# Performance work log

Hardware: AMD Instinct MI355X
Metric: run time of the kernel (lower is better)

The kernel has to match this reference:

```python
import jax, jax.numpy as jnp
import numpy as np

T = 2048      # sequence length (single unbatched sequence)
V = 32000     # vocab
D = 1024      # d_model
E = 16        # number of experts (one structural group)
TOPK = 2      # router top-k
CAP = 256     # per-expert capacity (T*TOPK/E)
DFF = 2048    # expert MLP hidden
NHOPS = 2     # number of routing hops
EPS = 1e-5    # RMSNorm eps


def setup_inputs() -> dict:
    key = jax.random.key(0)
    ks = jax.random.split(key, 6)
    ids = jax.random.randint(ks[0], (T,), 0, V)
    embed_W = jax.random.normal(ks[1], (V, D), jnp.float32) * 0.02
    ln_scale = jnp.ones((D,), jnp.float32)
    router_W = jax.random.normal(ks[2], (NHOPS, D, E), jnp.float32) * (D ** -0.5)
    expert_W1 = jax.random.normal(ks[3], (NHOPS, E, D, DFF), jnp.float32) * (D ** -0.5)
    expert_W2 = jax.random.normal(ks[4], (NHOPS, E, DFF, D), jnp.float32) * (DFF ** -0.5)
    return dict(ids=ids, embed_W=embed_W, ln_scale=ln_scale,
                router_W=router_W, expert_W1=expert_W1, expert_W2=expert_W2)


def _hop(h, Wr, W1, W2):
    # Router: clean logits -> mixing probs (softmax) + hard top-k selection mask.
    logits = h @ Wr                                   # (T, E)
    probs = jax.nn.softmax(logits, axis=-1)           # (T, E)
    _, top = jax.lax.top_k(logits, TOPK)              # (T, TOPK)
    mask = jnp.zeros((T, E), bool).at[jnp.arange(T)[:, None], top].set(True)

    # _capacity_select: rank tokens per expert by clean logits, keep top CAP.
    m = mask.T                                        # (E, T)
    g = jnp.where(m, logits.T, -jnp.inf)              # (E, T)
    _, top_idx = jax.lax.top_k(g, CAP)                # (E, C)
    slot = jnp.zeros((E, CAP, T), h.dtype)
    slot = slot.at[jnp.arange(E)[:, None], jnp.arange(CAP)[None, :], top_idx].set(1.0)
    slot = slot * m[:, None, :].astype(h.dtype)       # zero slots filled from -inf
    kept = slot.sum(1) > 0                            # (E, T)

    # One-hot einsum gather of token states into expert slot buffers.
    xin = jnp.einsum('ect,td->ecd', slot, h)          # (E, C, D)

    # Stable sort slots by original token position (active slots first).
    active = slot.sum(-1) > 0                         # (E, C)
    pos = jnp.where(active, top_idx, T + 1)
    order = jnp.argsort(pos, axis=1, stable=True)     # (E, C)
    xin = jnp.take_along_axis(xin, order[:, :, None], axis=1)
    slot = jnp.take_along_axis(slot, order[:, :, None], axis=1)

    # Grouped (stacked/vmapped) expert execution: GELU MLP per expert.
    h1 = jax.nn.gelu(jnp.einsum('ecd,edf->ecf', xin, W1))
    expert_out = jnp.einsum('ecf,efd->ecd', h1, W2)   # (E, C, D)

    # Combine (Eq. 3): h_{s+1} = h_s + sum_e rho_e (M_e(h) - h)
    cw = jnp.where(kept.T, probs, 0.0)                # (T, E)
    rho = cw.sum(axis=1, keepdims=True)               # (T, 1)
    combine = jnp.einsum('ecd,ect,et->td', expert_out, slot, cw.T)
    return h + combine - rho * h


def reference(ids, embed_W, ln_scale, router_W, expert_W1, expert_W2):
    h = embed_W[ids]                                  # (T, D) embedding lookup
    for i in range(NHOPS):
        h = _hop(h, router_W[i], expert_W1[i], expert_W2[i])
    # RMSNorm + tied unembedding
    h = h * jax.lax.rsqrt(jnp.mean(h * h, axis=-1, keepdims=True) + EPS) * ln_scale
    return h @ embed_W.T                              # (T, V)
```

## Files before the change

kernel.cpp:

```cpp
#include <hip/hip_runtime.h>
#include <stdint.h>

#define T_ 2048
#define V_ 32000
#define D_ 1024
#define E_ 16
#define CAP_ 256
#define DFF_ 2048

typedef unsigned short u16;
typedef unsigned int u32;
typedef __bf16 bf16x8 __attribute__((ext_vector_type(8)));
typedef float f32x4 __attribute__((ext_vector_type(4)));

__device__ __forceinline__ u16 f2bf(float f){
  u32 u = __float_as_uint(f);
  u32 r = u + 0x7FFFu + ((u >> 16) & 1u);
  return (u16)(r >> 16);
}
__device__ __forceinline__ float bf2f(u16 s){ return __uint_as_float(((u32)s) << 16); }

__device__ __forceinline__ void gl_lds16(const void* g, void* l){
  __builtin_amdgcn_global_load_lds((const __attribute__((address_space(1))) void*)g,
                                   (__attribute__((address_space(3))) void*)l, 16, 0, 0);
}
__device__ __forceinline__ f32x4 mfma16(bf16x8 a, bf16x8 b, f32x4 c){
  return __builtin_amdgcn_mfma_f32_16x16x32_bf16(a, b, c, 0, 0, 0);
}
__device__ __forceinline__ float gelu_tanh(float x){
  float u = 0.7978845608028654f * (x + 0.044715f * x * x * x);
  return 0.5f * x * (1.0f + tanhf(u));
}

__global__ __launch_bounds__(256) void k_cvtw(const float* __restrict__ W, u16* __restrict__ Wb){
  size_t i = ((size_t)blockIdx.x*256 + threadIdx.x)*8;
  float4 a = *(const float4*)(W + i);
  float4 b = *(const float4*)(W + i + 4);
  union { u16 s[8]; uint4 v; } p;
  p.s[0]=f2bf(a.x); p.s[1]=f2bf(a.y); p.s[2]=f2bf(a.z); p.s[3]=f2bf(a.w);
  p.s[4]=f2bf(b.x); p.s[5]=f2bf(b.y); p.s[6]=f2bf(b.z); p.s[7]=f2bf(b.w);
  *(uint4*)(Wb + i) = p.v;
}

template<bool EMB>
__global__ __launch_bounds__(256) void k_router(float* __restrict__ h,
    const float* __restrict__ Wr, float* __restrict__ logits,
    unsigned char* __restrict__ mask, int* __restrict__ top2, float* __restrict__ p2,
    const int* __restrict__ ids, const float* __restrict__ embW, int* __restrict__ etok){
  if (blockIdx.x < (E_*CAP_)/256) etok[blockIdx.x*256 + threadIdx.x] = -1;
  int w = threadIdx.x >> 6, l = threadIdx.x & 63;
  int t = blockIdx.x*4 + w;
  float acc[E_];
  #pragma unroll
  for (int e=0;e<E_;++e) acc[e]=0.f;
  const float* hrow = EMB ? (embW + (size_t)ids[t]*D_) : (h + (size_t)t*D_);
  #pragma unroll
  for (int i=0;i<16;++i){
    int d = l + i*64;
    float hv = hrow[d];
    if (EMB) h[(size_t)t*D_ + d] = hv;
    const float4* wr = (const float4*)(Wr + d*E_);
    float4 w0=wr[0], w1=wr[1], w2=wr[2], w3=wr[3];
    acc[0]+=hv*w0.x; acc[1]+=hv*w0.y; acc[2]+=hv*w0.z; acc[3]+=hv*w0.w;
    acc[4]+=hv*w1.x; acc[5]+=hv*w1.y; acc[6]+=hv*w1.z; acc[7]+=hv*w1.w;
    acc[8]+=hv*w2.x; acc[9]+=hv*w2.y; acc[10]+=hv*w2.z; acc[11]+=hv*w2.w;
    acc[12]+=hv*w3.x; acc[13]+=hv*w3.y; acc[14]+=hv*w3.z; acc[15]+=hv*w3.w;
  }
  #pragma unroll
  for (int off=32; off; off>>=1){
    #pragma unroll
    for (int e=0;e<E_;++e) acc[e] += __shfl_xor(acc[e], off, 64);
  }
  float mx = acc[0];
  #pragma unroll
  for (int e=1;e<E_;++e) mx = fmaxf(mx, acc[e]);
  float p[E_], s = 0.f;
  #pragma unroll
  for (int e=0;e<E_;++e){ p[e] = expf(acc[e]-mx); s += p[e]; }
  int i1 = 0; float v1 = acc[0];
  #pragma unroll
  for (int e=1;e<E_;++e) if (acc[e] > v1){ v1 = acc[e]; i1 = e; }
  int i2 = (i1==0)?1:0; float v2 = acc[i2];
  #pragma unroll
  for (int e=0;e<E_;++e) if (e!=i1 && e!=i2 && acc[e] > v2){ v2 = acc[e]; i2 = e; }
  if (l < E_){
    logits[t*E_+l] = acc[l];
    mask[t*E_+l] = (l==i1 || l==i2) ? 1 : 0;
  }
  if (l == 0){
    float inv = 1.f/s;
    top2[t*2] = i1; top2[t*2+1] = i2;
    p2[t*2] = p[i1]*inv; p2[t*2+1] = p[i2]*inv;
  }
}

__global__ __launch_bounds__(256) void k_capacity(const float* __restrict__ logits,
    const unsigned char* __restrict__ mask, const int* __restrict__ top2,
    int* __restrict__ kept, int* __restrict__ etok){
  int w = threadIdx.x >> 6, l = threadIdx.x & 63;
  int wid = blockIdx.x*4 + w;
  int t = wid >> 1, k = wid & 1;
  int e = top2[t*2+k];
  float my = logits[t*E_+e];
  int cnt = 0;
  for (int t2 = l; t2 < T_; t2 += 64){
    if (mask[t2*E_+e]){
      float lg = logits[t2*E_+e];
      if (lg > my || (lg == my && t2 < t)) cnt++;
    }
  }
  #pragma unroll
  for (int off=32; off; off>>=1) cnt += __shfl_xor(cnt, off, 64);
  if (l == 0){
    if (cnt < CAP_){ kept[t*2+k] = cnt; etok[e*CAP_+cnt] = t; }
    else kept[t*2+k] = -1;
  }
}

template<bool SPLIT>
__global__ __launch_bounds__(256) void k_gather(const float* __restrict__ h,
    const int* __restrict__ etok, u16* __restrict__ xhi, u16* __restrict__ xlo){
  int rc = blockIdx.x;
  int tok = etok[rc];
  int d = threadIdx.x * 4;
  float4 v = make_float4(0.f,0.f,0.f,0.f);
  if (tok >= 0) v = *(const float4*)(h + (size_t)tok*D_ + d);
  union { u16 s[4]; uint2 u; } hi, lo;
  hi.s[0]=f2bf(v.x); lo.s[0]=f2bf(v.x - bf2f(hi.s[0]));
  hi.s[1]=f2bf(v.y); lo.s[1]=f2bf(v.y - bf2f(hi.s[1]));
  hi.s[2]=f2bf(v.z); lo.s[2]=f2bf(v.z - bf2f(hi.s[2]));
  hi.s[3]=f2bf(v.w); lo.s[3]=f2bf(v.w - bf2f(hi.s[3]));
  *(uint2*)(xhi + (size_t)rc*D_ + d) = hi.u;
  if (SPLIT) *(uint2*)(xlo + (size_t)rc*D_ + d) = lo.u;
}

template<bool SPLIT, bool GELU, int BN>
__global__ __launch_bounds__(512, 4) void k_expert(
    const u16* __restrict__ Ahi, const u16* __restrict__ Alo,
    const float* __restrict__ Bw,
    u16* __restrict__ Ohi, u16* __restrict__ Olo, float* __restrict__ Of,
    int N, int K){
  constexpr int NI = BN/64;
  constexpr int ASLOT = 8192;
  constexpr int ABYTES = 2*ASLOT*(SPLIT?2:1);
  constexpr int BSLOT = BN*80;
  constexpr int BBYTES = 2*BSLOT*(SPLIT?2:1);
  __shared__ __align__(16) char sm[ABYTES + BBYTES];
  char* smA   = sm;
  char* smALo = sm + 2*ASLOT;
  char* smB   = sm + ABYTES;
  char* smBLo = sm + ABYTES + 2*BSLOT;

  int bid = blockIdx.x;
  int swz = (bid & 7)*64 + (bid >> 3);
  int e   = swz >> 5;
  int rem = swz & 31;
  int mt  = rem & 1;
  int nt  = rem >> 1;
  int n0  = nt * BN;
  int tid = threadIdx.x;
  int lane = tid & 63;
  int w = tid >> 6;
  int wm = w >> 2, wn = w & 3;
  int lr = lane & 15, lq = lane >> 4;
  int NK = K >> 5;

  const u16* Ah = Ahi + ((size_t)e*256 + mt*128)*K;
  const u16* Al = SPLIT ? (Alo + ((size_t)e*256 + mt*128)*K) : (const u16*)nullptr;
  const float* Bb = Bw + (size_t)e*K*N + n0;

  f32x4 acc[4][NI];
  #pragma unroll
  for (int i=0;i<4;++i)
    #pragma unroll
    for (int j=0;j<NI;++j)
      #pragma unroll
      for (int c=0;c<4;++c) acc[i][j][c] = 0.f;

  int t2 = tid - 256;
  const u16* aSrcH[2]; const u16* aSrcL[2]; int aDst[2];
  #pragma unroll
  for (int r=0;r<2;++r){
    int o = r*4096 + t2*16;
    int row = o >> 6;
    int cs = ((o >> 4) & 3) ^ ((row >> 1) & 3);
    aDst[r] = o;
    aSrcH[r] = Ah + (size_t)row*K + cs*8;
    if (SPLIT) aSrcL[r] = Al + (size_t)row*K + cs*8;
  }
  int kb = (BN==128) ? (tid>>5) : (tid>>4);
  int nb = (BN==128) ? (tid&31) : (tid&15);
  int wOff[4];
  #pragma unroll
  for (int j=0;j<4;++j){
    int n = nb*4 + j;
    int pos;
    if (BN==128) pos = ((kb ^ (2*(nb&3))) & 7) * 8;
    else         pos = (kb*4) ^ ((nb&3)*16);
    wOff[j] = n*80 + pos;
  }
  float4 pb[4];

  #define LOADPB_(k0n) do { \
    if constexpr (BN==128){ \
      const float* bp = Bb + (size_t)((k0n) + kb*4)*N + nb*4; \
      pb[0] = *(const float4*)bp; pb[1] = *(const float4*)(bp + N); \
      pb[2] = *(const float4*)(bp + 2*N); pb[3] = *(const float4*)(bp + 3*N); \
    } else { \
      const float* bp = Bb + (size_t)((k0n) + kb*2)*N + nb*4; \
      pb[0] = *(const float4*)bp; pb[1] = *(const float4*)(bp + N); \
    } } while(0)

  #define WRITEB_(slot) do { \
    char* bh_ = smB + (slot)*BSLOT; char* bl_ = smBLo + (slot)*BSLOT; \
    if constexpr (BN==128){ \
      float cv[4][4] = {{pb[0].x,pb[1].x,pb[2].x,pb[3].x},{pb[0].y,pb[1].y,pb[2].y,pb[3].y}, \
                        {pb[0].z,pb[1].z,pb[2].z,pb[3].z},{pb[0].w,pb[1].w,pb[2].w,pb[3].w}}; \
      _Pragma("unroll") for (int j=0;j<4;++j){ \
        union { u16 s[4]; uint2 u; } hi, lo; \
        _Pragma("unroll") for (int i=0;i<4;++i){ \
          hi.s[i] = f2bf(cv[j][i]); \
          if constexpr (SPLIT) lo.s[i] = f2bf(cv[j][i] - bf2f(hi.s[i])); } \
        *(uint2*)(bh_ + wOff[j]) = hi.u; \
        if constexpr (SPLIT) *(uint2*)(bl_ + wOff[j]) = lo.u; } \
    } else { \
      float cv[4][2] = {{pb[0].x,pb[1].x},{pb[0].y,pb[1].y},{pb[0].z,pb[1].z},{pb[0].w,pb[1].w}}; \
      _Pragma("unroll") for (int j=0;j<4;++j){ \
        union { u16 s[2]; u32 u; } hi, lo; \
        _Pragma("unroll") for (int i=0;i<2;++i){ \
          hi.s[i] = f2bf(cv[j][i]); \
          if constexpr (SPLIT) lo.s[i] = f2bf(cv[j][i] - bf2f(hi.s[i])); } \
        *(u32*)(bh_ + wOff[j]) = hi.u; \
        if constexpr (SPLIT) *(u32*)(bl_ + wOff[j]) = lo.u; } \
    } } while(0)

  #define STAGEA_(k0n, slot) do { \
    _Pragma("unroll") for (int r=0;r<2;++r){ \
      gl_lds16(aSrcH[r] + (k0n), smA + (slot)*ASLOT + aDst[r]); \
      if constexpr (SPLIT) gl_lds16(aSrcL[r] + (k0n), smALo + (slot)*ASLOT + aDst[r]); \
    } } while(0)

  if (tid < 256){
    LOADPB_(0);
    WRITEB_(0);
    if (NK > 1) LOADPB_(32);
  } else {
    STAGEA_(0, 0);
  }
  __syncthreads();

  int aRo[4];
  #pragma unroll
  for (int mi=0;mi<4;++mi){
    int row = wm*64 + mi*16 + lr;
    aRo[mi] = row*64 + ((lq ^ ((row>>1)&3))<<4);
  }
  int bRo[NI];
  #pragma unroll
  for (int ni=0;ni<NI;++ni){
    int n = wn*(BN/4) + ni*16 + lr;
    bRo[ni] = n*80 + ((lq ^ ((n>>2)&3))<<4);
  }

  for (int ks = 0; ks < NK; ++ks){
    int cur = ks & 1;
    bf16x8 bh[NI], bl[NI];
    #pragma unroll
    for (int ni=0;ni<NI;++ni){
      bh[ni] = *(const bf16x8*)(smB + cur*BSLOT + bRo[ni]);
      if constexpr (SPLIT) bl[ni] = *(const bf16x8*)(smBLo + cur*BSLOT + bRo[ni]);
    }
    if (ks + 1 < NK){
      int nslot = cur ^ 1;
      if (tid < 256){
        WRITEB_(nslot);
        if (ks + 2 < NK) LOADPB_((ks+2)*32);
      } else {
        STAGEA_((ks+1)*32, nslot);
      }
    }
    #pragma unroll
    for (int mi=0;mi<4;++mi){
      bf16x8 ah = *(const bf16x8*)(smA + cur*ASLOT + aRo[mi]);
      if constexpr (SPLIT){
        bf16x8 al = *(const bf16x8*)(smALo + cur*ASLOT + aRo[mi]);
        #pragma unroll
        for (int ni=0;ni<NI;++ni){
          acc[mi][ni] = mfma16(ah, bh[ni], acc[mi][ni]);
          acc[mi][ni] = mfma16(al, bh[ni], acc[mi][ni]);
          acc[mi][ni] = mfma16(ah, bl[ni], acc[mi][ni]);
        }
      } else {
        #pragma unroll
        for (int ni=0;ni<NI;++ni)
          acc[mi][ni] = mfma16(ah, bh[ni], acc[mi][ni]);
      }
    }
    __syncthreads();
  }
  #undef LOADPB_
  #undef WRITEB_
  #undef STAGEA_

  {
    constexpr int STRIPB = NI*16*4*16;
    char* strip = sm + w*STRIPB;
    int r = lane & 15;
    int b = lane >> 4;
    #pragma unroll
    for (int mi=0;mi<4;++mi){
      #pragma unroll
      for (int ni=0;ni<NI;++ni){
        int col = ni*16 + lr;
        f32x4 v = acc[mi][ni];
        if constexpr (GELU){
          v[0]=gelu_tanh(v[0]); v[1]=gelu_tanh(v[1]);
          v[2]=gelu_tanh(v[2]); v[3]=gelu_tanh(v[3]);
        }
        *(f32x4*)(strip + (col*4 + lq)*16) = v;
      }
      asm volatile("s_waitcnt lgkmcnt(0)" ::: "memory");
      __builtin_amdgcn_sched_barrier(0);
      int grow = mt*128 + wm*64 + mi*16 + r;
      if constexpr (GELU){
        union { u16 s[8]; uint4 v; } ph, pl;
        #pragma unroll
        for (int i=0;i<8;++i){
          float y = *(const float*)(strip + ((b*8+i)*4 + (r>>2))*16 + (r&3)*4);
          ph.s[i] = f2bf(y);
          if constexpr (SPLIT) pl.s[i] = f2bf(y - bf2f(ph.s[i]));
        }
        size_t idx = ((size_t)e*256 + grow)*N + n0 + wn*(BN/4) + b*8;
        *(uint4*)(Ohi + idx) = ph.v;
        if constexpr (SPLIT) *(uint4*)(Olo + idx) = pl.v;
      } else {
        #pragma unroll
        for (int cc=0; cc<NI; ++cc){
          int c = b + cc*4;
          float4 o;
          o.x = *(const float*)(strip + ((c*4+0)*4 + (r>>2))*16 + (r&3)*4);
          o.y = *(const float*)(strip + ((c*4+1)*4 + (r>>2))*16 + (r&3)*4);
          o.z = *(const float*)(strip + ((c*4+2)*4 + (r>>2))*16 + (r&3)*4);
          o.w = *(const float*)(strip + ((c*4+3)*4 + (r>>2))*16 + (r&3)*4);
          *(float4*)(Of + ((size_t)e*256 + grow)*N + n0 + wn*(BN/4) + c*4) = o;
        }
      }
      asm volatile("s_waitcnt lgkmcnt(0)" ::: "memory");
    }
  }
}

template<bool FINAL>
__global__ __launch_bounds__(256) void k_combine(float* __restrict__ h,
    const float* __restrict__ Y2, const int* __restrict__ top2,
    const float* __restrict__ p2, const int* __restrict__ kept,
    const float* __restrict__ g, u16* __restrict__ hn){
  int t = blockIdx.x;
  int e0 = top2[t*2], e1 = top2[t*2+1];
  int r0 = kept[t*2], r1 = kept[t*2+1];
  float w0 = (r0 >= 0) ? p2[t*2]   : 0.f;
  float w1 = (r1 >= 0) ? p2[t*2+1] : 0.f;
  float om = 1.f - w0 - w1;
  int d = threadIdx.x * 4;
  float4 v = *(const float4*)(h + (size_t)t*D_ + d);
  float ox = v.x*om, oy = v.y*om, oz = v.z*om, ow = v.w*om;
  if (r0 >= 0){
    float4 y = *(const float4*)(Y2 + ((size_t)e0*CAP_ + r0)*D_ + d);
    ox += w0*y.x; oy += w0*y.y; oz += w0*y.z; ow += w0*y.w;
  }
  if (r1 >= 0){
    float4 y = *(const float4*)(Y2 + ((size_t)e1*CAP_ + r1)*D_ + d);
    ox += w1*y.x; oy += w1*y.y; oz += w1*y.z; ow += w1*y.w;
  }
  if constexpr (!FINAL){
    *(float4*)(h + (size_t)t*D_ + d) = make_float4(ox, oy, oz, ow);
  } else {
    int w = threadIdx.x >> 6, l = threadIdx.x & 63;
    __shared__ float red[4];
    float ss = ox*ox + oy*oy + oz*oz + ow*ow;
    #pragma unroll
    for (int off=32; off; off>>=1) ss += __shfl_xor(ss, off, 64);
    if (l == 0) red[w] = ss;
    __syncthreads();
    float tot = red[0] + red[1] + red[2] + red[3];
    float sc = rsqrtf(tot * (1.f/D_) + 1e-5f);
    float4 gs = *(const float4*)(g + d);
    union { u16 s[4]; uint2 u; } o;
    o.s[0] = f2bf(ox*sc*gs.x); o.s[1] = f2bf(oy*sc*gs.y);
    o.s[2] = f2bf(oz*sc*gs.z); o.s[3] = f2bf(ow*sc*gs.w);
    *(uint2*)(hn + (size_t)t*D_ + d) = o.u;
  }
}

#define SLOT_ 16384
__global__ __launch_bounds__(512, 2) void k_gemm_final(const u16* __restrict__ A,
    const u16* __restrict__ B, float* __restrict__ C){
  __shared__ __align__(16) char lds[131072];
  char* ldsA = lds;
  char* ldsB = lds + 65536;
  int bid = blockIdx.x;
  int wgid = (bid & 7) * 125 + (bid >> 3);
  int m0 = (wgid & 7) << 8;
  int n0 = (wgid >> 3) << 8;
  int tid = threadIdx.x;
  int lane = tid & 63;
  int w = tid >> 6;
  int wm = w >> 2, wn = w & 3;
  int lr = lane & 15, lq = lane >> 4;

  f32x4 acc[8][4];
  #pragma unroll
  for (int i=0;i<8;++i)
    #pragma unroll
    for (int j=0;j<4;++j)
      #pragma unroll
      for (int c=0;c<4;++c) acc[i][j][c] = 0.f;

  int j_0 = w*2, j_1 = w*2 + 1;
  int rp0 = j_0*8 + (lane>>3), rp1 = j_1*8 + (lane>>3);
  int c80 = (lane&7) ^ (rp0&7), c81 = (lane&7) ^ (rp1&7);
  int rA0 = rp0*2 + (c80>>2), rA1 = rp1*2 + (c81>>2);
  int cc0 = (c80&3)*8,        cc1 = (c81&3)*8;
  const u16* sA0 = A + (size_t)(m0+rA0)*D_ + cc0;
  const u16* sA1 = A + (size_t)(m0+rA1)*D_ + cc1;
  const u16* sB0 = B + (size_t)(n0+rA0)*D_ + cc0;
  const u16* sB1 = B + (size_t)(n0+rA1)*D_ + cc1;
  int d0 = j_0*1024 + lane*16, d1 = j_1*1024 + lane*16;

  int aoff[8], boff[4];
  #pragma unroll
  for (int mi=0;mi<8;++mi){
    int r = wm*128 + mi*16 + lr;
    int rp = r >> 1;
    int c8 = ((r&1)<<2) | lq;
    aoff[mi] = rp*128 + ((c8 ^ (rp&7))<<4);
  }
  #pragma unroll
  for (int ni=0;ni<4;++ni){
    int r = wn*64 + ni*16 + lr;
    int rp = r >> 1;
    int c8 = ((r&1)<<2) | lq;
    boff[ni] = rp*128 + ((c8 ^ (rp&7))<<4);
  }

  #define STAGE_(sbase) do { \
    gl_lds16(sA0, ldsA + (sbase) + d0); gl_lds16(sB0, ldsB + (sbase) + d0); \
    gl_lds16(sA1, ldsA + (sbase) + d1); gl_lds16(sB1, ldsB + (sbase) + d1); \
    sA0 += 32; sA1 += 32; sB0 += 32; sB1 += 32; } while(0)

  bf16x8 aF0[8], bF0[4], aF1[8], bF1[4];

  STAGE_(0); STAGE_(SLOT_); STAGE_(2*SLOT_);
  asm volatile("s_waitcnt vmcnt(8)" ::: "memory");
  __builtin_amdgcn_s_barrier();
  {
    const char* pA_ = ldsA; const char* pB_ = ldsB;
    #pragma unroll
    for (int ni=0;ni<4;++ni) bF0[ni] = *(const bf16x8*)(pB_ + boff[ni]);
    #pragma unroll
    for (int mi=0;mi<8;++mi) aF0[mi] = *(const bf16x8*)(pA_ + aoff[mi]);
  }

  #define PHASE_(kh, FAc, FBc, FAn, FBn) do { \
    if ((kh) <= 28) STAGE_((((kh)+3)&3)*SLOT_); \
    if ((kh) <= 28)      asm volatile("s_waitcnt vmcnt(8)" ::: "memory"); \
    else if ((kh) == 29) asm volatile("s_waitcnt vmcnt(4)" ::: "memory"); \
    else if ((kh) == 30) asm volatile("s_waitcnt vmcnt(0)" ::: "memory"); \
    asm volatile("s_waitcnt lgkmcnt(0)" ::: "memory"); \
    __builtin_amdgcn_sched_barrier(0); \
    __builtin_amdgcn_s_barrier(); \
    __builtin_amdgcn_sched_barrier(0); \
    if ((kh) < 31){ \
      int sb_ = (((kh)+1)&3)*SLOT_; \
      const char* pA_ = ldsA + sb_; const char* pB_ = ldsB + sb_; \
      _Pragma("unroll") for (int ni=0;ni<4;++ni) FBn[ni] = *(const bf16x8*)(pB_ + boff[ni]); \
      _Pragma("unroll") for (int mi=0;mi<8;++mi) FAn[mi] = *(const bf16x8*)(pA_ + aoff[mi]); \
    } \
    __builtin_amdgcn_s_setprio(1); \
    _Pragma("unroll") for (int mi=0;mi<8;++mi){ \
      _Pragma("unroll") for (int ni=0;ni<4;++ni) \
        acc[mi][ni] = mfma16(FAc[mi], FBc[ni], acc[mi][ni]); \
    } \
    __builtin_amdgcn_s_setprio(0); \
  } while(0)

  for (int kh2 = 0; kh2 < 32; kh2 += 2){
    PHASE_(kh2,     aF0, bF0, aF1, bF1);
    PHASE_(kh2 + 1, aF1, bF1, aF0, bF0);
  }
  #undef PHASE_
  #undef STAGE_

  #pragma unroll
  for (int mi=0;mi<8;++mi)
    #pragma unroll
    for (int ni=0;ni<4;++ni)
      #pragma unroll
      for (int j=0;j<4;++j){
        int row = m0 + wm*128 + mi*16 + lq*4 + j;
        int col = n0 + wn*64 + ni*16 + lr;
        C[(size_t)row * V_ + col] = acc[mi][ni][j];
      }
}

extern "C" void kernel_launch(void* const* d_in, const int* in_sizes, int n_in,
                              void* d_out, int out_size, void* d_ws, size_t ws_size,
                              hipStream_t stream){
  const int*   ids  = (const int*)d_in[0];
  const float* embW = (const float*)d_in[1];
  const float* lns  = (const float*)d_in[2];
  const float* WrA  = (const float*)d_in[3];
  const float* W1A  = (const float*)d_in[4];
  const float* W2A  = (const float*)d_in[5];
  float* out = (float*)d_out;
  char* ws = (char*)d_ws;
  const size_t MB = 1u << 20;

  float* h      = (float*)(ws);
  float* logits = (float*)(ws + 8*MB);
  unsigned char* mask = (unsigned char*)(ws + 8*MB + 131072);
  int*   top2v  = (int*)(ws + 8*MB + 131072 + 32768);
  float* p2     = (float*)(ws + 8*MB + 131072 + 32768 + 16384);
  int*   kept   = (int*)(ws + 8*MB + 131072 + 32768 + 32768);
  int*   etok   = (int*)(ws + 8*MB + 131072 + 32768 + 49152);
  u16*   xhi  = (u16*)(ws + 9*MB);
  u16*   xlo  = (u16*)(ws + 17*MB);
  float* y2   = (float*)(ws + 9*MB);
  u16*   y1hi = (u16*)(ws + 25*MB);
  u16*   y1lo = (u16*)(ws + 41*MB);
  u16*   hn   = (u16*)(ws + 57*MB);
  u16*   ebf  = (u16*)(ws + 61*MB);

  k_cvtw<<<(V_*D_)/(256*8), 256, 0, stream>>>(embW, ebf);

  for (int hop = 0; hop < 2; ++hop){
    const float* Wr = WrA + (size_t)hop*D_*E_;
    const float* W1 = W1A + (size_t)hop*E_*D_*DFF_;
    const float* W2 = W2A + (size_t)hop*E_*DFF_*D_;
    if (hop == 0){
      k_router<true ><<<T_/4, 256, 0, stream>>>(h, Wr, logits, mask, top2v, p2, ids, embW, etok);
      k_capacity<<<T_*2/4, 256, 0, stream>>>(logits, mask, top2v, kept, etok);
      k_gather<true ><<<E_*CAP_, 256, 0, stream>>>(h, etok, xhi, xlo);
      k_expert<true , true , 128><<<E_*2*(DFF_/128), 512, 0, stream>>>(
          xhi, xlo, W1, y1hi, y1lo, nullptr, DFF_, D_);
      k_expert<true , false, 64 ><<<E_*2*(D_/64), 512, 0, stream>>>(
          y1hi, y1lo, W2, nullptr, nullptr, y2, D_, DFF_);
      k_combine<false><<<T_, 256, 0, stream>>>(h, y2, top2v, p2, kept, lns, hn);
    } else {
      k_router<false><<<T_/4, 256, 0, stream>>>(h, Wr, logits, mask, top2v, p2, ids, embW, etok);
      k_capacity<<<T_*2/4, 256, 0, stream>>>(logits, mask, top2v, kept, etok);
      k_gather<false><<<E_*CAP_, 256, 0, stream>>>(h, etok, xhi, xlo);
      k_expert<false, true , 128><<<E_*2*(DFF_/128), 512, 0, stream>>>(
          xhi, nullptr, W1, y1hi, nullptr, nullptr, DFF_, D_);
      k_expert<false, false, 64 ><<<E_*2*(D_/64), 512, 0, stream>>>(
          y1hi, nullptr, W2, nullptr, nullptr, y2, D_, DFF_);
      k_combine<true ><<<T_, 256, 0, stream>>>(h, y2, top2v, p2, kept, lns, hn);
    }
  }

  k_gemm_final<<<(T_/256)*(V_/256), 512, 0, stream>>>(hn, ebf, out);
}
```

Baseline: 548.9 us.

## Triple-buffer A tiles and fix expert GEMM tile width at 64

The expert GEMM kernel drops the BN template and always uses 64-column tiles, so the first expert GEMM launches twice as many blocks. The A operand moves to a three-slot LDS ring that is staged two k-steps ahead. __syncthreads is replaced by explicit vmcnt/lgkmcnt waits plus s_barrier, so global-to-LDS loads can stay in flight across iterations. The aim is better overlap of memory traffic with MFMA work and more blocks to fill the device, at the cost of less B reuse per block and more total A traffic.

Result: slower. 572.3 us (+4.3%).

```diff
diff --git a/kernel.cpp b/kernel.cpp
--- a/kernel.cpp
+++ b/kernel.cpp
@@ -134,30 +134,30 @@
   if (SPLIT) *(uint2*)(xlo + (size_t)rc*D_ + d) = lo.u;
 }
 
-template<bool SPLIT, bool GELU, int BN>
+template<bool SPLIT, bool GELU>
 __global__ __launch_bounds__(512, 4) void k_expert(
     const u16* __restrict__ Ahi, const u16* __restrict__ Alo,
     const float* __restrict__ Bw,
     u16* __restrict__ Ohi, u16* __restrict__ Olo, float* __restrict__ Of,
     int N, int K){
-  constexpr int NI = BN/64;
   constexpr int ASLOT = 8192;
-  constexpr int ABYTES = 2*ASLOT*(SPLIT?2:1);
-  constexpr int BSLOT = BN*80;
-  constexpr int BBYTES = 2*BSLOT*(SPLIT?2:1);
-  __shared__ __align__(16) char sm[ABYTES + BBYTES];
+  constexpr int BSLOT = 64*80;
+  constexpr int NA = SPLIT ? 2 : 1;
+  __shared__ __align__(16) char sm[3*ASLOT*NA + 2*BSLOT*NA];
   char* smA   = sm;
-  char* smALo = sm + 2*ASLOT;
-  char* smB   = sm + ABYTES;
-  char* smBLo = sm + ABYTES + 2*BSLOT;
-
+  char* smALo = sm + 3*ASLOT;
+  char* smB   = sm + 3*ASLOT*NA;
+  char* smBLo = smB + 2*BSLOT;
+
+  int chunk = gridDim.x >> 3;
   int bid = blockIdx.x;
-  int swz = (bid & 7)*64 + (bid >> 3);
-  int e   = swz >> 5;
-  int rem = swz & 31;
+  int swz = (bid & 7)*chunk + (bid >> 3);
+  int tpe = N >> 5;
+  int e   = swz / tpe;
+  int rem = swz - e*tpe;
   int mt  = rem & 1;
   int nt  = rem >> 1;
-  int n0  = nt * BN;
+  int n0  = nt * 64;
   int tid = threadIdx.x;
   int lane = tid & 63;
   int w = tid >> 6;
@@ -169,13 +169,11 @@
   const u16* Al = SPLIT ? (Alo + ((size_t)e*256 + mt*128)*K) : (const u16*)nullptr;
   const float* Bb = Bw + (size_t)e*K*N + n0;
 
-  f32x4 acc[4][NI];
+  f32x4 acc[4];
   #pragma unroll
   for (int i=0;i<4;++i)
     #pragma unroll
-    for (int j=0;j<NI;++j)
-      #pragma unroll
-      for (int c=0;c<4;++c) acc[i][j][c] = 0.f;
+    for (int c=0;c<4;++c) acc[i][c] = 0.f;
 
   int t2 = tid - 256;
   const u16* aSrcH[2]; const u16* aSrcL[2]; int aDst[2];
@@ -188,51 +186,32 @@
     aSrcH[r] = Ah + (size_t)row*K + cs*8;
     if (SPLIT) aSrcL[r] = Al + (size_t)row*K + cs*8;
   }
-  int kb = (BN==128) ? (tid>>5) : (tid>>4);
-  int nb = (BN==128) ? (tid&31) : (tid&15);
+  int kb = tid >> 4;
+  int nb = tid & 15;
   int wOff[4];
   #pragma unroll
   for (int j=0;j<4;++j){
     int n = nb*4 + j;
-    int pos;
-    if (BN==128) pos = ((kb ^ (2*(nb&3))) & 7) * 8;
-    else         pos = (kb*4) ^ ((nb&3)*16);
-    wOff[j] = n*80 + pos;
-  }
-  float4 pb[4];
+    wOff[j] = n*80 + ((kb*4) ^ ((nb&3)*16));
+  }
+  float4 pb[2];
 
   #define LOADPB_(k0n) do { \
-    if constexpr (BN==128){ \
-      const float* bp = Bb + (size_t)((k0n) + kb*4)*N + nb*4; \
-      pb[0] = *(const float4*)bp; pb[1] = *(const float4*)(bp + N); \
-      pb[2] = *(const float4*)(bp + 2*N); pb[3] = *(const float4*)(bp + 3*N); \
-    } else { \
-      const float* bp = Bb + (size_t)((k0n) + kb*2)*N + nb*4; \
-      pb[0] = *(const float4*)bp; pb[1] = *(const float4*)(bp + N); \
-    } } while(0)
+    const float* bp = Bb + (size_t)((k0n) + kb*2)*N + nb*4; \
+    pb[0] = *(const float4*)bp; pb[1] = *(const float4*)(bp + N); \
+  } while(0)
 
   #define WRITEB_(slot) do { \
     char* bh_ = smB + (slot)*BSLOT; char* bl_ = smBLo + (slot)*BSLOT; \
-    if constexpr (BN==128){ \
-      float cv[4][4] = {{pb[0].x,pb[1].x,pb[2].x,pb[3].x},{pb[0].y,pb[1].y,pb[2].y,pb[3].y}, \
-                        {pb[0].z,pb[1].z,pb[2].z,pb[3].z},{pb[0].w,pb[1].w,pb[2].w,pb[3].w}}; \
-      _Pragma("unroll") for (int j=0;j<4;++j){ \
-        union { u16 s[4]; uint2 u; } hi, lo; \
-        _Pragma("unroll") for (int i=0;i<4;++i){ \
-          hi.s[i] = f2bf(cv[j][i]); \
-          if constexpr (SPLIT) lo.s[i] = f2bf(cv[j][i] - bf2f(hi.s[i])); } \
-        *(uint2*)(bh_ + wOff[j]) = hi.u; \
-        if constexpr (SPLIT) *(uint2*)(bl_ + wOff[j]) = lo.u; } \
-    } else { \
-      float cv[4][2] = {{pb[0].x,pb[1].x},{pb[0].y,pb[1].y},{pb[0].z,pb[1].z},{pb[0].w,pb[1].w}}; \
-      _Pragma("unroll") for (int j=0;j<4;++j){ \
-        union { u16 s[2]; u32 u; } hi, lo; \
-        _Pragma("unroll") for (int i=0;i<2;++i){ \
-          hi.s[i] = f2bf(cv[j][i]); \
-          if constexpr (SPLIT) lo.s[i] = f2bf(cv[j][i] - bf2f(hi.s[i])); } \
-        *(u32*)(bh_ + wOff[j]) = hi.u; \
-        if constexpr (SPLIT) *(u32*)(bl_ + wOff[j]) = lo.u; } \
-    } } while(0)
+    float cv[4][2] = {{pb[0].x,pb[1].x},{pb[0].y,pb[1].y},{pb[0].z,pb[1].z},{pb[0].w,pb[1].w}}; \
+    _Pragma("unroll") for (int j=0;j<4;++j){ \
+      union { u16 s[2]; u32 u; } hi, lo; \
+      _Pragma("unroll") for (int i=0;i<2;++i){ \
+        hi.s[i] = f2bf(cv[j][i]); \
+        if constexpr (SPLIT) lo.s[i] = f2bf(cv[j][i] - bf2f(hi.s[i])); } \
+      *(u32*)(bh_ + wOff[j]) = hi.u; \
+      if constexpr (SPLIT) *(u32*)(bl_ + wOff[j]) = lo.u; } \
+  } while(0)
 
   #define STAGEA_(k0n, slot) do { \
     _Pragma("unroll") for (int r=0;r<2;++r){ \
@@ -240,14 +219,18 @@
       if constexpr (SPLIT) gl_lds16(aSrcL[r] + (k0n), smALo + (slot)*ASLOT + aDst[r]); \
     } } while(0)
 
-  if (tid < 256){
+  if (tid >= 256){
+    STAGEA_(0, 0);
+    STAGEA_(32, 1);
+  } else {
     LOADPB_(0);
     WRITEB_(0);
-    if (NK > 1) LOADPB_(32);
-  } else {
-    STAGEA_(0, 0);
-  }
-  __syncthreads();
+    LOADPB_(32);
+  }
+  if (SPLIT) asm volatile("s_waitcnt vmcnt(4)" ::: "memory");
+  else       asm volatile("s_waitcnt vmcnt(2)" ::: "memory");
+  asm volatile("s_waitcnt lgkmcnt(0)" ::: "memory");
+  __builtin_amdgcn_s_barrier();
 
   int aRo[4];
   #pragma unroll
@@ -255,95 +238,76 @@
     int row = wm*64 + mi*16 + lr;
     aRo[mi] = row*64 + ((lq ^ ((row>>1)&3))<<4);
   }
-  int bRo[NI];
-  #pragma unroll
-  for (int ni=0;ni<NI;++ni){
-    int n = wn*(BN/4) + ni*16 + lr;
-    bRo[ni] = n*80 + ((lq ^ ((n>>2)&3))<<4);
-  }
+  int bn = wn*16 + lr;
+  int bRo = bn*80 + ((lq ^ ((bn>>2)&3))<<4);
 
   for (int ks = 0; ks < NK; ++ks){
-    int cur = ks & 1;
-    bf16x8 bh[NI], bl[NI];
-    #pragma unroll
-    for (int ni=0;ni<NI;++ni){
-      bh[ni] = *(const bf16x8*)(smB + cur*BSLOT + bRo[ni]);
-      if constexpr (SPLIT) bl[ni] = *(const bf16x8*)(smBLo + cur*BSLOT + bRo[ni]);
+    if (tid >= 256){
+      if (ks + 2 < NK) STAGEA_((ks+2)*32, (ks+2)%3);
+    } else {
+      if (ks + 1 < NK) WRITEB_((ks+1)&1);
+      if (ks + 2 < NK) LOADPB_((ks+2)*32);
     }
-    if (ks + 1 < NK){
-      int nslot = cur ^ 1;
-      if (tid < 256){
-        WRITEB_(nslot);
-        if (ks + 2 < NK) LOADPB_((ks+2)*32);
+    int cA = (ks%3)*ASLOT, cB = (ks&1)*BSLOT;
+    bf16x8 bh = *(const bf16x8*)(smB + cB + bRo);
+    bf16x8 bl;
+    if constexpr (SPLIT) bl = *(const bf16x8*)(smBLo + cB + bRo);
+    #pragma unroll
+    for (int mi=0;mi<4;++mi){
+      bf16x8 ah = *(const bf16x8*)(smA + cA + aRo[mi]);
+      if constexpr (SPLIT){
+        bf16x8 al = *(const bf16x8*)(smALo + cA + aRo[mi]);
+        acc[mi] = mfma16(ah, bh, acc[mi]);
+        acc[mi] = mfma16(al, bh, acc[mi]);
+        acc[mi] = mfma16(ah, bl, acc[mi]);
       } else {
-        STAGEA_((ks+1)*32, nslot);
+        acc[mi] = mfma16(ah, bh, acc[mi]);
       }
     }
-    #pragma unroll
-    for (int mi=0;mi<4;++mi){
-      bf16x8 ah = *(const bf16x8*)(smA + cur*ASLOT + aRo[mi]);
-      if constexpr (SPLIT){
-        bf16x8 al = *(const bf16x8*)(smALo + cur*ASLOT + aRo[mi]);
-        #pragma unroll
-        for (int ni=0;ni<NI;++ni){
-          acc[mi][ni] = mfma16(ah, bh[ni], acc[mi][ni]);
-          acc[mi][ni] = mfma16(al, bh[ni], acc[mi][ni]);
-          acc[mi][ni] = mfma16(ah, bl[ni], acc[mi][ni]);
-        }
-      } else {
-        #pragma unroll
-        for (int ni=0;ni<NI;++ni)
-          acc[mi][ni] = mfma16(ah, bh[ni], acc[mi][ni]);
-      }
+    if (ks + 2 < NK){
+      if (SPLIT) asm volatile("s_waitcnt vmcnt(4)" ::: "memory");
+      else       asm volatile("s_waitcnt vmcnt(2)" ::: "memory");
+    } else {
+      asm volatile("s_waitcnt vmcnt(0)" ::: "memory");
     }
-    __syncthreads();
+    asm volatile("s_waitcnt lgkmcnt(0)" ::: "memory");
+    __builtin_amdgcn_s_barrier();
   }
   #undef LOADPB_
   #undef WRITEB_
   #undef STAGEA_
 
   {
-    constexpr int STRIPB = NI*16*4*16;
-    char* strip = sm + w*STRIPB;
+    char* strip = sm + w*1024;
     int r = lane & 15;
     int b = lane >> 4;
     #pragma unroll
     for (int mi=0;mi<4;++mi){
-      #pragma unroll
-      for (int ni=0;ni<NI;++ni){
-        int col = ni*16 + lr;
-        f32x4 v = acc[mi][ni];
-        if constexpr (GELU){
-          v[0]=gelu_tanh(v[0]); v[1]=gelu_tanh(v[1]);
-          v[2]=gelu_tanh(v[2]); v[3]=gelu_tanh(v[3]);
-        }
-        *(f32x4*)(strip + (col*4 + lq)*16) = v;
+      f32x4 v = acc[mi];
+      if constexpr (GELU){
+        v[0]=gelu_tanh(v[0]); v[1]=gelu_tanh(v[1]);
+        v[2]=gelu_tanh(v[2]); v[3]=gelu_tanh(v[3]);
       }
+      *(f32x4*)(strip + (lr*4 + lq)*16) = v;
       asm volatile("s_waitcnt lgkmcnt(0)" ::: "memory");
       __builtin_amdgcn_sched_barrier(0);
       int grow = mt*128 + wm*64 + mi*16 + r;
+      float o0 = *(const float*)(strip + (((b*4+0)*4 + (r>>2))*16) + (r&3)*4);
+      float o1 = *(const float*)(strip + (((b*4+1)*4 + (r>>2))*16) + (r&3)*4);
+      float o2 = *(const float*)(strip + (((b*4+2)*4 + (r>>2))*16) + (r&3)*4);
+      float o3 = *(const float*)(strip + (((b*4+3)*4 + (r>>2))*16) + (r&3)*4);
+      size_t idx = ((size_t)e*256 + grow)*N + n0 + wn*16 + b*4;
       if constexpr (GELU){
-        union { u16 s[8]; uint4 v; } ph, pl;
-        #pragma unroll
-        for (int i=0;i<8;++i){
-          float y = *(const float*)(strip + ((b*8+i)*4 + (r>>2))*16 + (r&3)*4);
-          ph.s[i] = f2bf(y);
-          if constexpr (SPLIT) pl.s[i] = f2bf(y - bf2f(ph.s[i]));
+        union { u16 s[4]; uint2 u; } ph, pl;
+        ph.s[0]=f2bf(o0); ph.s[1]=f2bf(o1); ph.s[2]=f2bf(o2); ph.s[3]=f2bf(o3);
+        if constexpr (SPLIT){
+          pl.s[0]=f2bf(o0-bf2f(ph.s[0])); pl.s[1]=f2bf(o1-bf2f(ph.s[1]));
+          pl.s[2]=f2bf(o2-bf2f(ph.s[2])); pl.s[3]=f2bf(o3-bf2f(ph.s[3]));
         }
-        size_t idx = ((size_t)e*256 + grow)*N + n0 + wn*(BN/4) + b*8;
-        *(uint4*)(Ohi + idx) = ph.v;
-        if constexpr (SPLIT) *(uint4*)(Olo + idx) = pl.v;
+        *(uint2*)(Ohi + idx) = ph.u;
+        if constexpr (SPLIT) *(uint2*)(Olo + idx) = pl.u;
       } else {
-        #pragma unroll
-        for (int cc=0; cc<NI; ++cc){
-          int c = b + cc*4;
-          float4 o;
-          o.x = *(const float*)(strip + ((c*4+0)*4 + (r>>2))*16 + (r&3)*4);
-          o.y = *(const float*)(strip + ((c*4+1)*4 + (r>>2))*16 + (r&3)*4);
-          o.z = *(const float*)(strip + ((c*4+2)*4 + (r>>2))*16 + (r&3)*4);
-          o.w = *(const float*)(strip + ((c*4+3)*4 + (r>>2))*16 + (r&3)*4);
-          *(float4*)(Of + ((size_t)e*256 + grow)*N + n0 + wn*(BN/4) + c*4) = o;
-        }
+        *(float4*)(Of + idx) = make_float4(o0, o1, o2, o3);
       }
       asm volatile("s_waitcnt lgkmcnt(0)" ::: "memory");
     }
@@ -541,18 +505,18 @@
       k_router<true ><<<T_/4, 256, 0, stream>>>(h, Wr, logits, mask, top2v, p2, ids, embW, etok);
       k_capacity<<<T_*2/4, 256, 0, stream>>>(logits, mask, top2v, kept, etok);
       k_gather<true ><<<E_*CAP_, 256, 0, stream>>>(h, etok, xhi, xlo);
-      k_expert<true , true , 128><<<E_*2*(DFF_/128), 512, 0, stream>>>(
+      k_expert<true , true ><<<E_*2*(DFF_/64), 512, 0, stream>>>(
           xhi, xlo, W1, y1hi, y1lo, nullptr, DFF_, D_);
-      k_expert<true , false, 64 ><<<E_*2*(D_/64), 512, 0, stream>>>(
+      k_expert<true , false><<<E_*2*(D_/64), 512, 0, stream>>>(
           y1hi, y1lo, W2, nullptr, nullptr, y2, D_, DFF_);
       k_combine<false><<<T_, 256, 0, stream>>>(h, y2, top2v, p2, kept, lns, hn);
     } else {
       k_router<false><<<T_/4, 256, 0, stream>>>(h, Wr, logits, mask, top2v, p2, ids, embW, etok);
       k_capacity<<<T_*2/4, 256, 0, stream>>>(logits, mask, top2v, kept, etok);
       k_gather<false><<<E_*CAP_, 256, 0, stream>>>(h, etok, xhi, xlo);
-      k_expert<false, true , 128><<<E_*2*(DFF_/128), 512, 0, stream>>>(
+      k_expert<false, true ><<<E_*2*(DFF_/64), 512, 0, stream>>>(
           xhi, nullptr, W1, y1hi, nullptr, nullptr, DFF_, D_);
-      k_expert<false, false, 64 ><<<E_*2*(D_/64), 512, 0, stream>>>(
+      k_expert<false, false><<<E_*2*(D_/64), 512, 0, stream>>>(
           y1hi, nullptr, W2, nullptr, nullptr, y2, D_, DFF_);
       k_combine<true ><<<T_, 256, 0, stream>>>(h, y2, top2v, p2, kept, lns, hn);
     }
```
